# Kernel optimization log

Hardware: AMD Instinct MI355X
Metric: run time of the kernel (lower is better)

Reference implementation:

```python
import jax, jax.numpy as jnp
import numpy as np

DIM = 384
HEADS = 12
WS = 7


def setup_inputs() -> dict:
    key = jax.random.key(0)
    ks = jax.random.split(key, 5)
    B, H, W = 16, 56, 56
    x = jax.random.normal(ks[0], (B, H * W, DIM), dtype=jnp.float32)
    # torch Linear weight (out,in) used as x @ W here, qkv_bias=False
    w_qkv = jax.random.normal(ks[1], (DIM, 3 * DIM), dtype=jnp.float32) * 0.02
    w_proj = jax.random.normal(ks[2], (DIM, DIM), dtype=jnp.float32) * 0.02
    b_proj = jax.random.normal(ks[3], (DIM,), dtype=jnp.float32) * 0.02
    # depthwise 3x3 conv (groups=dim): HWIO kernel (3,3,1,DIM), bias=True
    w_conv = jax.random.normal(ks[4], (3, 3, 1, DIM), dtype=jnp.float32) * 0.02
    b_conv = jnp.zeros((DIM,), jnp.float32)
    return {"x": x, "w_qkv": w_qkv, "w_proj": w_proj, "b_proj": b_proj,
            "w_conv": w_conv, "b_conv": b_conv, "H": H, "W": W}


def reference(x, w_qkv, w_proj, b_proj, w_conv, b_conv, H, W):
    B, N, C = x.shape
    hd = C // HEADS
    scale = hd ** (-0.5)
    hg, wg = H // WS, W // WS  # H,W chosen divisible by ws (no-pad fast path)

    qkv = x @ w_qkv  # (B, N, 3C)
    q, k, v = jnp.split(qkv, 3, axis=-1)

    def to_win(t):
        # (B,N,C) -> (B, n_windows, heads, ws*ws, head_dim)
        t = t.reshape(B, hg, WS, wg, WS, HEADS, hd)
        return t.transpose(0, 1, 3, 5, 2, 4, 6).reshape(B, hg * wg, HEADS, WS * WS, hd)

    qw, kw, vw = to_win(q), to_win(k), to_win(v)

    attn = jax.nn.softmax(jnp.einsum('bwhqd,bwhkd->bwhqk', qw, kw) * scale, axis=-1)
    out = jnp.einsum('bwhqk,bwhkd->bwhqd', attn, vw)
    # merge windows back: (B,nw,heads,q,d) -> (B,N,C)
    out = out.reshape(B, hg, wg, HEADS, WS, WS, hd)
    out = out.transpose(0, 1, 4, 2, 5, 3, 6).reshape(B, N, C)

    # LIM: win2img(img2win(v)) is just v as (B,C,H,W); depthwise 3x3 conv
    v_img = v.reshape(B, H, W, C).transpose(0, 3, 1, 2)
    v_lim = jax.lax.conv_general_dilated(
        v_img, w_conv, window_strides=(1, 1), padding='SAME',
        dimension_numbers=('NCHW', 'HWIO', 'NCHW'), feature_group_count=C)
    v_lim = v_lim + b_conv[None, :, None, None]
    v_lim = v_lim.reshape(B, C, N).transpose(0, 2, 1)  # (B, N, C)

    out = out + v_lim
    return out @ w_proj + b_proj
```

## Files before the change

### kernel.cpp

```cpp
#include <hip/hip_runtime.h>
#include <cstdint>
#include <cstddef>

typedef __bf16 bf16x8 __attribute__((ext_vector_type(8)));
typedef float floatx4 __attribute__((ext_vector_type(4)));

#define DEV static __device__ __forceinline__

DEV float bf2f(uint16_t u) {
    union { uint32_t i; float f; } x; x.i = ((uint32_t)u) << 16; return x.f;
}
DEV uint16_t f2bf(float f) {
    uint32_t u = __float_as_uint(f);
    uint32_t r = (u + 0x7FFFu + ((u >> 16) & 1u)) >> 16;
    return (uint16_t)r;
}
DEV bf16x8 as_bf8(uint4 u) {
    union { uint4 u; bf16x8 b; } c; c.u = u; return c.b;
}
DEV void g2l16(const void* g, void* l) {
    __builtin_amdgcn_global_load_lds(
        (const __attribute__((address_space(1))) void*)g,
        (__attribute__((address_space(3))) void*)l, 16, 0, 0);
}

union U16x8 { uint16_t h[8]; uint4 u; };

constexpr int DIMC  = 384;
constexpr int HEADS = 12;
constexpr int IMH   = 56, IMW = 56;
constexpr int NTOK  = IMH * IMW;
constexpr int BATCH = 16;
constexpr int MTOT  = BATCH * NTOK;
constexpr int QKVLD = 3 * DIMC;
constexpr int GK    = 384;

__global__ __launch_bounds__(256) void cvt_bf16(const float* __restrict__ in,
                                                uint16_t* __restrict__ out)
{
    size_t i = ((size_t)blockIdx.x * 256 + threadIdx.x) * 8;
    float4 a = *(const float4*)(in + i);
    float4 b = *(const float4*)(in + i + 4);
    U16x8 t;
    t.h[0] = f2bf(a.x); t.h[1] = f2bf(a.y); t.h[2] = f2bf(a.z); t.h[3] = f2bf(a.w);
    t.h[4] = f2bf(b.x); t.h[5] = f2bf(b.y); t.h[6] = f2bf(b.z); t.h[7] = f2bf(b.w);
    *(uint4*)(out + i) = t.u;
}

__global__ __launch_bounds__(256) void transpose_cvt(const float* __restrict__ in,
                                                     uint16_t* __restrict__ out,
                                                     int R, int C)
{
    int idx = blockIdx.x * 256 + threadIdx.x;
    int r = idx % R, c = idx / R;
    out[idx] = f2bf(in[(size_t)r * C + c]);
}

template<bool CF32>
__global__ __launch_bounds__(256) void gemm_bt(const uint16_t* __restrict__ A,
                                               const uint16_t* __restrict__ Bt,
                                               const float* __restrict__ bias,
                                               void* __restrict__ Cptr,
                                               int N)
{
    __shared__ __align__(16) uint16_t sA[128 * 32];
    __shared__ __align__(16) uint16_t sB[128 * 32];

    const int t    = threadIdx.x;
    const int bm   = blockIdx.x, bn = blockIdx.y;
    const int wave = t >> 6, lane = t & 63;
    const int wm   = (wave >> 1) * 64, wn = (wave & 1) * 64;
    const int lr   = lane & 15, quad = lane >> 4;

    const uint16_t* Ag = A  + (size_t)(bm * 128 + (t >> 2)) * GK + (t & 3) * 8;
    const uint16_t* Bg = Bt + (size_t)(bn * 128 + (t >> 2)) * GK + (t & 3) * 8;
    uint16_t* lA1 = sA + wave * 512;
    uint16_t* lA2 = sA + 2048 + wave * 512;
    uint16_t* lB1 = sB + wave * 512;
    uint16_t* lB2 = sB + 2048 + wave * 512;

    floatx4 acc[4][4] = {};

    #pragma unroll
    for (int k0 = 0; k0 < GK; k0 += 32) {
        __syncthreads();
        g2l16(Ag + k0, lA1);
        g2l16(Ag + (size_t)64 * GK + k0, lA2);
        g2l16(Bg + k0, lB1);
        g2l16(Bg + (size_t)64 * GK + k0, lB2);
        __syncthreads();

        bf16x8 af[4], bfr[4];
        #pragma unroll
        for (int mt = 0; mt < 4; ++mt)
            af[mt] = *(const bf16x8*)&sA[(wm + mt * 16 + lr) * 32 + quad * 8];
        #pragma unroll
        for (int nt = 0; nt < 4; ++nt)
            bfr[nt] = *(const bf16x8*)&sB[(wn + nt * 16 + lr) * 32 + quad * 8];
        #pragma unroll
        for (int mt = 0; mt < 4; ++mt)
            #pragma unroll
            for (int nt = 0; nt < 4; ++nt)
                acc[mt][nt] = __builtin_amdgcn_mfma_f32_16x16x32_bf16(
                    af[mt], bfr[nt], acc[mt][nt], 0, 0, 0);
    }

    #pragma unroll
    for (int mt = 0; mt < 4; ++mt) {
        #pragma unroll
        for (int nt = 0; nt < 4; ++nt) {
            int gc = bn * 128 + wn + nt * 16 + lr;
            float bv = bias ? bias[gc] : 0.0f;
            int gr0 = bm * 128 + wm + mt * 16 + quad * 4;
            #pragma unroll
            for (int i = 0; i < 4; ++i) {
                if constexpr (CF32) {
                    ((float*)Cptr)[(size_t)(gr0 + i) * N + gc] = acc[mt][nt][i] + bv;
                } else {
                    ((uint16_t*)Cptr)[(size_t)(gr0 + i) * N + gc] = f2bf(acc[mt][nt][i] + bv);
                }
            }
        }
    }
}

constexpr int PLD = 72;

__global__ __launch_bounds__(128) void attn_mfma(const uint16_t* __restrict__ qkv,
                                                 uint16_t* __restrict__ y)
{
    __shared__ uint16_t lds[2][(64 + 32) * PLD];

    const int wave = threadIdx.x >> 6;
    const int lane = threadIdx.x & 63;
    const int unit = blockIdx.x * 2 + wave;
    const int h  = unit % HEADS;
    const int w  = (unit / HEADS) & 63;
    const int b  = unit / (HEADS * 64);
    const int wy = w >> 3, wx = w & 7;
    const int lr = lane & 15, quad = lane >> 4;

    uint16_t* Pbuf = lds[wave];
    uint16_t* Vt   = lds[wave] + 64 * PLD;

    auto rowbase = [&](int i, int which) -> const uint16_t* {
        int py = i / 7, px = i % 7;
        int n = (wy * 7 + py) * IMW + wx * 7 + px;
        return qkv + (size_t)(b * NTOK + n) * QKVLD + which * DIMC + h * 32;
    };

    uint4 qf[4], kf[4];
    #pragma unroll
    for (int tm = 0; tm < 4; ++tm) {
        int i = tm * 16 + lr;
        if (i < 49) {
            qf[tm] = *(const uint4*)(rowbase(i, 0) + quad * 8);
            kf[tm] = *(const uint4*)(rowbase(i, 1) + quad * 8);
        } else {
            qf[tm] = uint4{0, 0, 0, 0};
            kf[tm] = uint4{0, 0, 0, 0};
        }
    }

    {
        int j = lane;
        uint16_t vrow[32];
        if (j < 49) {
            const uint16_t* vr = rowbase(j, 2);
            #pragma unroll
            for (int p = 0; p < 4; ++p) {
                U16x8 tmp; tmp.u = *(const uint4*)(vr + p * 8);
                #pragma unroll
                for (int q = 0; q < 8; ++q) vrow[p * 8 + q] = tmp.h[q];
            }
        } else {
            #pragma unroll
            for (int d = 0; d < 32; ++d) vrow[d] = 0;
        }
        #pragma unroll
        for (int d = 0; d < 32; ++d) Vt[d * PLD + j] = vrow[d];
    }

    floatx4 S[4][4] = {};
    #pragma unroll
    for (int tm = 0; tm < 4; ++tm)
        #pragma unroll
        for (int tn = 0; tn < 4; ++tn)
            S[tm][tn] = __builtin_amdgcn_mfma_f32_16x16x32_bf16(
                as_bf8(qf[tm]), as_bf8(kf[tn]), S[tm][tn], 0, 0, 0);

    const float scale = 0.17677669529663687f;
    const bool v3 = (lr == 0);
    #pragma unroll
    for (int tm = 0; tm < 4; ++tm) {
        #pragma unroll
        for (int i = 0; i < 4; ++i) {
            float e0 = __expf(S[tm][0][i] * scale);
            float e1 = __expf(S[tm][1][i] * scale);
            float e2 = __expf(S[tm][2][i] * scale);
            float e3 = v3 ? __expf(S[tm][3][i] * scale) : 0.0f;
            float s = e0 + e1 + e2 + e3;
            #pragma unroll
            for (int d = 1; d < 16; d <<= 1) s += __shfl_xor(s, d);
            float inv = 1.0f / s;
            int row = tm * 16 + quad * 4 + i;
            Pbuf[row * PLD + lr]      = f2bf(e0 * inv);
            Pbuf[row * PLD + 16 + lr] = f2bf(e1 * inv);
            Pbuf[row * PLD + 32 + lr] = f2bf(e2 * inv);
            Pbuf[row * PLD + 48 + lr] = f2bf(e3 * inv);
        }
    }

    floatx4 O[4][2] = {};
    #pragma unroll
    for (int kk = 0; kk < 2; ++kk) {
        bf16x8 pf[4], vf[2];
        #pragma unroll
        for (int tm = 0; tm < 4; ++tm)
            pf[tm] = *(const bf16x8*)&Pbuf[(tm * 16 + lr) * PLD + kk * 32 + quad * 8];
        #pragma unroll
        for (int tn = 0; tn < 2; ++tn)
            vf[tn] = *(const bf16x8*)&Vt[(tn * 16 + lr) * PLD + kk * 32 + quad * 8];
        #pragma unroll
        for (int tm = 0; tm < 4; ++tm)
            #pragma unroll
            for (int tn = 0; tn < 2; ++tn)
                O[tm][tn] = __builtin_amdgcn_mfma_f32_16x16x32_bf16(
                    pf[tm], vf[tn], O[tm][tn], 0, 0, 0);
    }

    #pragma unroll
    for (int tm = 0; tm < 4; ++tm) {
        #pragma unroll
        for (int i = 0; i < 4; ++i) {
            int r = tm * 16 + quad * 4 + i;
            if (r < 49) {
                int py = r / 7, px = r % 7;
                int n = (wy * 7 + py) * IMW + wx * 7 + px;
                uint16_t* dst = y + (size_t)(b * NTOK + n) * DIMC + h * 32;
                dst[lr]      = f2bf(O[tm][0][i]);
                dst[16 + lr] = f2bf(O[tm][1][i]);
            }
        }
    }
}

__global__ __launch_bounds__(256) void conv_kernel(const uint16_t* __restrict__ qkv,
                                                   const float* __restrict__ wconv,
                                                   const float* __restrict__ bconv,
                                                   uint16_t* __restrict__ y)
{
    constexpr int C8 = DIMC / 8;
    size_t idx = (size_t)blockIdx.x * 256 + threadIdx.x;
    int c8  = (int)(idx % C8);
    int rem = (int)(idx / C8);
    int n   = rem % NTOK;
    int b   = rem / NTOK;
    int c   = c8 * 8;
    int y0 = n / IMW, x0 = n % IMW;

    float acc[8];
    {
        float4 b0 = *(const float4*)(bconv + c);
        float4 b1 = *(const float4*)(bconv + c + 4);
        acc[0] = b0.x; acc[1] = b0.y; acc[2] = b0.z; acc[3] = b0.w;
        acc[4] = b1.x; acc[5] = b1.y; acc[6] = b1.z; acc[7] = b1.w;
    }

    const uint16_t* vbase = qkv + 2 * DIMC + c;
    #pragma unroll
    for (int ky = 0; ky < 3; ++ky) {
        int yy = y0 + ky - 1;
        if (yy < 0 || yy >= IMH) continue;
        #pragma unroll
        for (int kx = 0; kx < 3; ++kx) {
            int xx = x0 + kx - 1;
            if (xx < 0 || xx >= IMW) continue;
            U16x8 v;
            v.u = *(const uint4*)(vbase + (size_t)(b * NTOK + yy * IMW + xx) * QKVLD);
            const float* wp = wconv + (ky * 3 + kx) * DIMC + c;
            float4 w0 = *(const float4*)(wp);
            float4 w1 = *(const float4*)(wp + 4);
            acc[0] += bf2f(v.h[0]) * w0.x;
            acc[1] += bf2f(v.h[1]) * w0.y;
            acc[2] += bf2f(v.h[2]) * w0.z;
            acc[3] += bf2f(v.h[3]) * w0.w;
            acc[4] += bf2f(v.h[4]) * w1.x;
            acc[5] += bf2f(v.h[5]) * w1.y;
            acc[6] += bf2f(v.h[6]) * w1.z;
            acc[7] += bf2f(v.h[7]) * w1.w;
        }
    }

    uint16_t* yp = y + (size_t)rem * DIMC + c;
    U16x8 yo; yo.u = *(const uint4*)yp;
    #pragma unroll
    for (int j = 0; j < 8; ++j) yo.h[j] = f2bf(bf2f(yo.h[j]) + acc[j]);
    *(uint4*)yp = yo.u;
}

extern "C" void kernel_launch(void* const* d_in, const int* in_sizes, int n_in,
                              void* d_out, int out_size, void* d_ws, size_t ws_size,
                              hipStream_t stream)
{
    const float* x      = (const float*)d_in[0];
    const float* w_qkv  = (const float*)d_in[1];
    const float* w_proj = (const float*)d_in[2];
    const float* b_proj = (const float*)d_in[3];
    const float* w_conv = (const float*)d_in[4];
    const float* b_conv = (const float*)d_in[5];
    float* out = (float*)d_out;

    char* ws = (char*)d_ws;
    uint16_t* qkv    = (uint16_t*)ws;
    uint16_t* xb     = (uint16_t*)(ws + 115605504);
    uint16_t* yb     = xb;
    uint16_t* wqkvT  = (uint16_t*)(ws + 115605504 + 38535168);
    uint16_t* wprojT = wqkvT + QKVLD * GK;

    cvt_bf16<<<dim3((MTOT * DIMC) / (8 * 256)), 256, 0, stream>>>(x, xb);
    transpose_cvt<<<dim3((GK * QKVLD) / 256), 256, 0, stream>>>(w_qkv, wqkvT, GK, QKVLD);
    transpose_cvt<<<dim3((GK * DIMC) / 256), 256, 0, stream>>>(w_proj, wprojT, GK, DIMC);

    gemm_bt<false><<<dim3(MTOT / 128, QKVLD / 128), 256, 0, stream>>>(
        xb, wqkvT, nullptr, qkv, QKVLD);

    attn_mfma<<<dim3(BATCH * 64 * HEADS / 2), 128, 0, stream>>>(qkv, yb);

    conv_kernel<<<dim3((MTOT * (DIMC / 8)) / 256), 256, 0, stream>>>(
        qkv, w_conv, b_conv, yb);

    gemm_bt<true><<<dim3(MTOT / 128, DIMC / 128), 256, 0, stream>>>(
        yb, wprojT, b_proj, out, DIMC);
}
```

Before: 341.7 us.

## Double-buffer GEMM LDS tiles and swizzle block order for L2 reuse

The bf16 GEMM kernel now uses two LDS buffers. It issues the global-to-LDS loads for the next K step before computing the current one, which replaces the two barriers per iteration with one. The 2D grid becomes a 1D grid remapped so that groups of 8 M-tiles sweep all N tiles, improving L2 reuse of the A rows. This doubles LDS use per block, which may lower occupancy, and the loop count is hardcoded to 12 steps (GK=384).

```diff
diff --git a/kernel.cpp b/kernel.cpp
--- a/kernel.cpp
+++ b/kernel.cpp
@@ -63,46 +63,55 @@
                                                void* __restrict__ Cptr,
                                                int N)
 {
-    __shared__ __align__(16) uint16_t sA[128 * 32];
-    __shared__ __align__(16) uint16_t sB[128 * 32];
+    __shared__ __align__(16) uint16_t sA[2][128 * 32];
+    __shared__ __align__(16) uint16_t sB[2][128 * 32];
 
     const int t    = threadIdx.x;
-    const int bm   = blockIdx.x, bn = blockIdx.y;
+    const int NB   = N >> 7;
+    const int bid  = blockIdx.x;
+    const int chunk = bid / (8 * NB);
+    const int r     = bid % (8 * NB);
+    const int bm    = chunk * 8 + (r & 7);
+    const int bn    = r >> 3;
     const int wave = t >> 6, lane = t & 63;
     const int wm   = (wave >> 1) * 64, wn = (wave & 1) * 64;
     const int lr   = lane & 15, quad = lane >> 4;
 
     const uint16_t* Ag = A  + (size_t)(bm * 128 + (t >> 2)) * GK + (t & 3) * 8;
     const uint16_t* Bg = Bt + (size_t)(bn * 128 + (t >> 2)) * GK + (t & 3) * 8;
-    uint16_t* lA1 = sA + wave * 512;
-    uint16_t* lA2 = sA + 2048 + wave * 512;
-    uint16_t* lB1 = sB + wave * 512;
-    uint16_t* lB2 = sB + 2048 + wave * 512;
+
+    auto stage = [&](int buf, int k0) {
+        g2l16(Ag + k0, sA[buf] + wave * 512);
+        g2l16(Ag + (size_t)64 * GK + k0, sA[buf] + 2048 + wave * 512);
+        g2l16(Bg + k0, sB[buf] + wave * 512);
+        g2l16(Bg + (size_t)64 * GK + k0, sB[buf] + 2048 + wave * 512);
+    };
 
     floatx4 acc[4][4] = {};
 
-    #pragma unroll
-    for (int k0 = 0; k0 < GK; k0 += 32) {
-        __syncthreads();
-        g2l16(Ag + k0, lA1);
-        g2l16(Ag + (size_t)64 * GK + k0, lA2);
-        g2l16(Bg + k0, lB1);
-        g2l16(Bg + (size_t)64 * GK + k0, lB2);
-        __syncthreads();
+    stage(0, 0);
+    __syncthreads();
+
+    #pragma unroll
+    for (int ks = 0; ks < 12; ++ks) {
+        const int cur = ks & 1;
+        if (ks < 11) stage(cur ^ 1, (ks + 1) * 32);
 
         bf16x8 af[4], bfr[4];
         #pragma unroll
         for (int mt = 0; mt < 4; ++mt)
-            af[mt] = *(const bf16x8*)&sA[(wm + mt * 16 + lr) * 32 + quad * 8];
+            af[mt] = *(const bf16x8*)&sA[cur][(wm + mt * 16 + lr) * 32 + quad * 8];
         #pragma unroll
         for (int nt = 0; nt < 4; ++nt)
-            bfr[nt] = *(const bf16x8*)&sB[(wn + nt * 16 + lr) * 32 + quad * 8];
+            bfr[nt] = *(const bf16x8*)&sB[cur][(wn + nt * 16 + lr) * 32 + quad * 8];
         #pragma unroll
         for (int mt = 0; mt < 4; ++mt)
             #pragma unroll
             for (int nt = 0; nt < 4; ++nt)
                 acc[mt][nt] = __builtin_amdgcn_mfma_f32_16x16x32_bf16(
                     af[mt], bfr[nt], acc[mt][nt], 0, 0, 0);
+
+        __syncthreads();
     }
 
     #pragma unroll
@@ -322,7 +331,7 @@
     transpose_cvt<<<dim3((GK * QKVLD) / 256), 256, 0, stream>>>(w_qkv, wqkvT, GK, QKVLD);
     transpose_cvt<<<dim3((GK * DIMC) / 256), 256, 0, stream>>>(w_proj, wprojT, GK, DIMC);
 
-    gemm_bt<false><<<dim3(MTOT / 128, QKVLD / 128), 256, 0, stream>>>(
+    gemm_bt<false><<<dim3((MTOT / 128) * (QKVLD / 128)), 256, 0, stream>>>(
         xb, wqkvT, nullptr, qkv, QKVLD);
 
     attn_mfma<<<dim3(BATCH * 64 * HEADS / 2), 128, 0, stream>>>(qkv, yb);
@@ -330,6 +339,6 @@
     conv_kernel<<<dim3((MTOT * (DIMC / 8)) / 256), 256, 0, stream>>>(
         qkv, w_conv, b_conv, yb);
 
-    gemm_bt<true><<<dim3(MTOT / 128, DIMC / 128), 256, 0, stream>>>(
+    gemm_bt<true><<<dim3((MTOT / 128) * (DIMC / 128)), 256, 0, stream>>>(
         yb, wprojT, b_proj, out, DIMC);
 }
```

Measured after the change: 327.6 us. 1.04x faster.
